# Kernel tuning notes

Hardware: AMD Instinct MI355X
Metric: run time of the kernel (lower is better)

Reference implementation:

```python
import jax, jax.numpy as jnp
import numpy as np

LN_EPS = 1e-5        # torch default LayerNorm eps
DEB_EPS = 1e-7       # deberta-v3 layer_norm_eps
ATT_SPAN = 256       # deberta-v3-base position_buckets -> pos_ebd_size
MAX_REL = 100        # config.max_relative_positions override


def _ln(x, g, b, eps):
    m = x.mean(-1, keepdims=True)
    v = jnp.var(x, axis=-1, keepdims=True)
    return (x - m) * jax.lax.rsqrt(v + eps) * g + b


def _lin(x, w, b):
    return x @ w.T + b


def _rel_buckets(L):
    # build_relative_position + make_log_bucket_position (bucket_size=256, max_position=100)
    rel = jnp.arange(L, dtype=jnp.int32)[:, None] - jnp.arange(L, dtype=jnp.int32)[None, :]
    mid = ATT_SPAN // 2
    sign = jnp.sign(rel)
    abs_pos = jnp.where((rel < mid) & (rel > -mid), mid - 1, jnp.abs(rel))
    log_pos = jnp.ceil(jnp.log(abs_pos.astype(jnp.float32) / mid)
                       / np.float32(np.log((MAX_REL - 1) / mid)) * (mid - 1)) + mid
    return jnp.where(abs_pos <= mid, rel, (log_pos * sign).astype(jnp.int32))


def _forward(ints, floats):
    type_ids, landmark_ids, mask = ints
    (xs, ys, zs, type_emb, landmark_emb, type_ln_g, type_ln_b, lm_ln_g, lm_ln_b,
     pos_w, pos_b, lt_in_w, lt_in_b, lt_out_w, lt_out_b, lt_ln1_g, lt_ln1_b,
     lt_ff1_w, lt_ff1_b, lt_ff2_w, lt_ff2_b, lt_ln2_g, lt_ln2_b,
     rel_emb, rel_ln_g, rel_ln_b, dq_w, dq_b, dk_w, dk_b, dv_w, dv_b,
     dao_w, dao_b, da_ln_g, da_ln_b, di_w, di_b, do_w, do_b, do_ln_g, do_ln_b,
     head_w, head_b) = floats

    # embeddings (padding_idx=0 -> zero row & zero grad) + layernorms + pos projection
    te = _ln(type_emb[type_ids] * (type_ids != 0)[..., None].astype(jnp.float32), type_ln_g, type_ln_b, LN_EPS)
    le = _ln(landmark_emb[landmark_ids] * (landmark_ids != 0)[..., None].astype(jnp.float32), lm_ln_g, lm_ln_b, LN_EPS)
    pe = _lin(jnp.stack([xs, ys, zs], -1), pos_w, pos_b)
    fts = jnp.concatenate([te, le, pe], -1)                  # [B,F,L,768]
    B, F, L, D = fts.shape
    h = fts.reshape(B * F, L, D)

    # --- nn.TransformerEncoderLayer over landmarks (post-norm, relu, nhead=1) ---
    q, k, v = jnp.split(_lin(h, lt_in_w, lt_in_b), 3, axis=-1)
    probs = jax.nn.softmax(jnp.einsum('bqd,bkd->bqk', q, k) / np.float32(np.sqrt(D)), axis=-1)
    attn = _lin(jnp.einsum('bqk,bkd->bqd', probs, v), lt_out_w, lt_out_b)
    h = _ln(h + attn, lt_ln1_g, lt_ln1_b, LN_EPS)
    ff = _lin(jax.nn.relu(_lin(h, lt_ff1_w, lt_ff1_b)), lt_ff2_w, lt_ff2_b)
    h = _ln(h + ff, lt_ln2_g, lt_ln2_b, LN_EPS)

    h = h.reshape(B, F, L, D).mean(2)                        # [B,F,768]

    # --- DebertaV2 layer over frames (disentangled attention, 1 head) ---
    m = mask[:, :, 0] > 0                                    # [B,F]
    q = _lin(h, dq_w, dq_b)
    k = _lin(h, dk_w, dk_b)
    v = _lin(h, dv_w, dv_b)
    scale = np.float32(np.sqrt(D * 3))                       # scale_factor = 1 + len({c2p,p2c})
    scores = jnp.einsum('bqd,bkd->bqk', q, k) / scale
    rel_ln = _ln(rel_emb, rel_ln_g, rel_ln_b, DEB_EPS)       # norm_rel_ebd='layer_norm'
    pos_q = _lin(rel_ln, dq_w, dq_b)                         # share_att_key=True
    pos_k = _lin(rel_ln, dk_w, dk_b)
    rel = _rel_buckets(F)                                    # [F,F]
    c2p_idx = jnp.clip(rel + ATT_SPAN, 0, 2 * ATT_SPAN - 1)
    c2p = jnp.einsum('bqd,rd->bqr', q, pos_k)                # [B,F,512]
    c2p = jnp.take_along_axis(c2p, jnp.broadcast_to(c2p_idx[None], (B, F, F)), axis=-1)
    p2c_idx = jnp.clip(-rel + ATT_SPAN, 0, 2 * ATT_SPAN - 1)
    p2c = jnp.einsum('bkd,rd->bkr', k, pos_q)                # [B,F,512]
    p2c = jnp.take_along_axis(p2c, jnp.broadcast_to(p2c_idx[None], (B, F, F)), axis=-1)
    scores = scores + (c2p + jnp.swapaxes(p2c, -1, -2)) / scale
    amask = m[:, :, None] & m[:, None, :]                    # XSoftmax mask
    probs = jax.nn.softmax(jnp.where(amask, scores, jnp.finfo(scores.dtype).min), axis=-1)
    probs = jnp.where(amask, probs, 0.0)
    ctx = jnp.einsum('bqk,bkd->bqd', probs, v)
    h = _ln(_lin(ctx, dao_w, dao_b) + h, da_ln_g, da_ln_b, DEB_EPS)
    inter = jax.nn.gelu(_lin(h, di_w, di_b), approximate=False)
    h = _ln(_lin(inter, do_w, do_b) + h, do_ln_g, do_ln_b, DEB_EPS)

    return _lin(h.mean(1), head_w, head_b)                   # [B,250]


def setup_inputs():
    ks = iter(jax.random.split(jax.random.key(0), 64))
    B, F, L, E, D, DF, NC = 8, 80, 100, 256, 768, 3072, 250
    def w(*shape):
        return jax.random.normal(next(ks), shape, dtype=jnp.float32) * 0.02
    z = lambda *s: jnp.zeros(s, jnp.float32)
    o = lambda *s: jnp.ones(s, jnp.float32)
    return {
        "type_ids": jax.random.randint(next(ks), (B, F, L), 0, 12, dtype=jnp.int32),
        "landmark_ids": jax.random.randint(next(ks), (B, F, L), 0, 127, dtype=jnp.int32),
        "xs": jax.random.normal(next(ks), (B, F, L), dtype=jnp.float32),
        "ys": jax.random.normal(next(ks), (B, F, L), dtype=jnp.float32),
        "zs": jax.random.normal(next(ks), (B, F, L), dtype=jnp.float32),
        "mask": jnp.ones((B, F, L), jnp.int32),
        "type_emb": w(12, E), "landmark_emb": w(127, E),
        "type_ln_g": o(E), "type_ln_b": z(E), "lm_ln_g": o(E), "lm_ln_b": z(E),
        "pos_w": w(E, 3), "pos_b": z(E),
        "lt_in_w": w(3 * D, D), "lt_in_b": z(3 * D), "lt_out_w": w(D, D), "lt_out_b": z(D),
        "lt_ln1_g": o(D), "lt_ln1_b": z(D),
        "lt_ff1_w": w(D, D), "lt_ff1_b": z(D), "lt_ff2_w": w(D, D), "lt_ff2_b": z(D),
        "lt_ln2_g": o(D), "lt_ln2_b": z(D),
        "rel_emb": w(2 * ATT_SPAN, D), "rel_ln_g": o(D), "rel_ln_b": z(D),
        "dq_w": w(D, D), "dq_b": z(D), "dk_w": w(D, D), "dk_b": z(D), "dv_w": w(D, D), "dv_b": z(D),
        "dao_w": w(D, D), "dao_b": z(D), "da_ln_g": o(D), "da_ln_b": z(D),
        "di_w": w(DF, D), "di_b": z(DF), "do_w": w(D, DF), "do_b": z(D),
        "do_ln_g": o(D), "do_ln_b": z(D),
        "head_w": w(NC, D), "head_b": z(NC),
    }


def reference(type_ids, landmark_ids, xs, ys, zs, mask, type_emb, landmark_emb,
              type_ln_g, type_ln_b, lm_ln_g, lm_ln_b, pos_w, pos_b,
              lt_in_w, lt_in_b, lt_out_w, lt_out_b, lt_ln1_g, lt_ln1_b,
              lt_ff1_w, lt_ff1_b, lt_ff2_w, lt_ff2_b, lt_ln2_g, lt_ln2_b,
              rel_emb, rel_ln_g, rel_ln_b, dq_w, dq_b, dk_w, dk_b, dv_w, dv_b,
              dao_w, dao_b, da_ln_g, da_ln_b, di_w, di_b, do_w, do_b,
              do_ln_g, do_ln_b, head_w, head_b):
    floats = (xs, ys, zs, type_emb, landmark_emb, type_ln_g, type_ln_b, lm_ln_g, lm_ln_b,
              pos_w, pos_b, lt_in_w, lt_in_b, lt_out_w, lt_out_b, lt_ln1_g, lt_ln1_b,
              lt_ff1_w, lt_ff1_b, lt_ff2_w, lt_ff2_b, lt_ln2_g, lt_ln2_b,
              rel_emb, rel_ln_g, rel_ln_b, dq_w, dq_b, dk_w, dk_b, dv_w, dv_b,
              dao_w, dao_b, da_ln_g, da_ln_b, di_w, di_b, do_w, do_b, do_ln_g, do_ln_b,
              head_w, head_b)
    return _forward((type_ids, landmark_ids, mask), floats)
```

## Files before the change

kernel.cpp:

```cpp
#include <hip/hip_runtime.h>

using short8v = __attribute__((ext_vector_type(8))) short;
using float4v = __attribute__((ext_vector_type(4))) float;

__device__ __forceinline__ unsigned short f2bf(float f) {
  unsigned int u = __float_as_uint(f);
  u += 0x7FFF + ((u >> 16) & 1);
  return (unsigned short)(u >> 16);
}
__device__ __forceinline__ float bf2f(unsigned short u) {
  return __uint_as_float((unsigned int)u << 16);
}

__device__ __forceinline__ int swz(int row, int c) {
  return row * 64 + (c ^ ((row & 7) << 3));
}

template<int BM, int ACT, bool OUTBF, int RES>
__global__ __launch_bounds__(256) void gemm_mfma(
    const unsigned short* __restrict__ A, const unsigned short* __restrict__ B,
    const float* __restrict__ bias, const void* __restrict__ resid, int ldr,
    void* __restrict__ Cv,
    int M, int N, int K, int lda, int ldb, int ldc,
    long long sA, long long sB, long long sC, long long sBias, float alpha)
{
  constexpr int NF = BM / 32;
  A += (long long)blockIdx.z * sA;
  B += (long long)blockIdx.z * sB;
  if (bias) bias += (long long)blockIdx.z * sBias;
  const int m0 = blockIdx.y * BM, n0 = blockIdx.x * BM;

  __shared__ __align__(16) unsigned short As[BM * 64];
  __shared__ __align__(16) unsigned short Bs[BM * 64];

  const int tid = threadIdx.x;
  const int w = tid >> 6, lane = tid & 63;
  const int wr = w >> 1, wc = w & 1;

  const int r0 = tid >> 3;
  const int c8 = (tid & 7) * 8;
  int ra[NF], rb[NF], soff[NF];
  #pragma unroll
  for (int i = 0; i < NF; ++i) {
    int r = m0 + r0 + i * 32; ra[i] = r < M - 1 ? r : M - 1;
    int q = n0 + r0 + i * 32; rb[i] = q < N - 1 ? q : N - 1;
    soff[i] = swz(r0 + i * 32, c8);
  }

  const int fr = lane & 15;
  const int fk = (lane >> 4) * 8;

  float4v acc[NF][NF] = {};

  short8v pa[NF], pb[NF];
  #pragma unroll
  for (int i = 0; i < NF; ++i) {
    pa[i] = *(const short8v*)(A + (long long)ra[i] * lda + c8);
    pb[i] = *(const short8v*)(B + (long long)rb[i] * ldb + c8);
  }

  for (int k0 = 0; k0 < K; k0 += 64) {
    __syncthreads();
    #pragma unroll
    for (int i = 0; i < NF; ++i) {
      *(short8v*)&As[soff[i]] = pa[i];
      *(short8v*)&Bs[soff[i]] = pb[i];
    }
    __syncthreads();
    if (k0 + 64 < K) {
      #pragma unroll
      for (int i = 0; i < NF; ++i) {
        pa[i] = *(const short8v*)(A + (long long)ra[i] * lda + k0 + 64 + c8);
        pb[i] = *(const short8v*)(B + (long long)rb[i] * ldb + k0 + 64 + c8);
      }
    }
    #pragma unroll
    for (int kk = 0; kk < 2; ++kk) {
      short8v a[NF], b[NF];
      #pragma unroll
      for (int i = 0; i < NF; ++i) {
        a[i] = *(const short8v*)&As[swz(wr * (NF * 16) + i * 16 + fr, kk * 32 + fk)];
        b[i] = *(const short8v*)&Bs[swz(wc * (NF * 16) + i * 16 + fr, kk * 32 + fk)];
      }
      #pragma unroll
      for (int mi = 0; mi < NF; ++mi)
        #pragma unroll
        for (int ni = 0; ni < NF; ++ni)
          acc[mi][ni] = __builtin_amdgcn_mfma_f32_16x16x32_bf16(a[mi], b[ni], acc[mi][ni], 0, 0, 0);
    }
  }

  const int ccol0 = n0 + wc * (NF * 16) + (lane & 15);
  const int crow0 = m0 + wr * (NF * 16) + (lane >> 4) * 4;
  float* Cf = (float*)Cv + (long long)blockIdx.z * sC;
  unsigned short* Cb = (unsigned short*)Cv + (long long)blockIdx.z * sC;
  #pragma unroll
  for (int ni = 0; ni < NF; ++ni) {
    const int col = ccol0 + ni * 16;
    if (col >= N) continue;
    const float bs = bias ? bias[col] : 0.f;
    #pragma unroll
    for (int mi = 0; mi < NF; ++mi) {
      #pragma unroll
      for (int r = 0; r < 4; ++r) {
        const int row = crow0 + mi * 16 + r;
        if (row >= M) continue;
        float v = acc[mi][ni][r] * alpha + bs;
        if (RES == 1) v += bf2f(((const unsigned short*)resid)[(long long)row * ldr + col]);
        if (RES == 2) v += ((const float*)resid)[(long long)row * ldr + col];
        if (ACT == 1) v = fmaxf(v, 0.f);
        if (ACT == 2) v = 0.5f * v * (1.f + erff(v * 0.70710678118654752f));
        if (OUTBF) Cb[(long long)row * ldc + col] = f2bf(v);
        else       Cf[(long long)row * ldc + col] = v;
      }
    }
  }
}

static void mg(hipStream_t st, int bm, int act, bool outbf, int res,
               const unsigned short* A, const unsigned short* B,
               const float* bias, const void* resid, int ldr, void* C,
               int M, int N, int K, int lda, int ldb, int ldc,
               long long sA, long long sB, long long sC, long long sBias,
               int bat, float alpha)
{
  dim3 grid((N + bm - 1) / bm, (M + bm - 1) / bm, bat);
  dim3 blk(256);
  #define GEMM_CALL(BM_, A_, O_, R_) \
    gemm_mfma<BM_, A_, O_, R_><<<grid, blk, 0, st>>>(A, B, bias, resid, ldr, C, \
        M, N, K, lda, ldb, ldc, sA, sB, sC, sBias, alpha)
  if (bm == 128) {
    if (outbf) {
      if (act == 1)       GEMM_CALL(128, 1, true, 0);
      else if (res == 1)  GEMM_CALL(128, 0, true, 1);
      else                GEMM_CALL(128, 0, true, 0);
    } else {
      GEMM_CALL(128, 0, false, 0);
    }
  } else {
    if (outbf) {
      if (act == 2)       GEMM_CALL(64, 2, true, 0);
      else                GEMM_CALL(64, 0, true, 0);
    } else {
      if (res == 2)       GEMM_CALL(64, 0, false, 2);
      else                GEMM_CALL(64, 0, false, 0);
    }
  }
  #undef GEMM_CALL
}

template<int MODE>
__global__ __launch_bounds__(256) void attn_fused(
    const unsigned short* __restrict__ Q, const unsigned short* __restrict__ Kp,
    const unsigned short* __restrict__ VT,
    const float* __restrict__ c2p, const float* __restrict__ p2c,
    const int* __restrict__ mask,
    unsigned short* __restrict__ O,
    int Mv, int K, int lda, int ldvt, int ldc,
    long long sQ, long long sVT, long long sO, float alpha)
{
  const int z = blockIdx.z;
  Q  += (long long)z * sQ;
  Kp += (long long)z * sQ;
  VT += (long long)z * sVT;
  O  += (long long)z * sO;

  __shared__ __align__(16) unsigned short As[128 * 64];
  __shared__ __align__(16) unsigned short Bs[128 * 64];
  __shared__ __align__(16) unsigned short Pl[128 * 128];
  float* ovl = (float*)As;
  int*   smk = (int*)(ovl + 512);

  const int tid = threadIdx.x;
  const int w = tid >> 6, lane = tid & 63;
  const int wr = w >> 1, wc = w & 1;
  const int r0 = tid >> 3, c8 = (tid & 7) * 8;

  int ra[4], soff[4];
  #pragma unroll
  for (int i = 0; i < 4; ++i) {
    int r = r0 + i * 32;
    ra[i] = (r < Mv - 1 ? r : Mv - 1);
    soff[i] = swz(r, c8);
  }
  const int fr = lane & 15, fk = (lane >> 4) * 8;

  float4v acc[4][4] = {};
  short8v pa[4], pb[4];
  #pragma unroll
  for (int i = 0; i < 4; ++i) {
    pa[i] = *(const short8v*)(Q  + (long long)ra[i] * lda + c8);
    pb[i] = *(const short8v*)(Kp + (long long)ra[i] * lda + c8);
  }
  for (int k0 = 0; k0 < K; k0 += 64) {
    __syncthreads();
    #pragma unroll
    for (int i = 0; i < 4; ++i) {
      *(short8v*)&As[soff[i]] = pa[i];
      *(short8v*)&Bs[soff[i]] = pb[i];
    }
    __syncthreads();
    if (k0 + 64 < K) {
      #pragma unroll
      for (int i = 0; i < 4; ++i) {
        pa[i] = *(const short8v*)(Q  + (long long)ra[i] * lda + k0 + 64 + c8);
        pb[i] = *(const short8v*)(Kp + (long long)ra[i] * lda + k0 + 64 + c8);
      }
    }
    #pragma unroll
    for (int kk = 0; kk < 2; ++kk) {
      short8v a[4], b[4];
      #pragma unroll
      for (int i = 0; i < 4; ++i) {
        a[i] = *(const short8v*)&As[swz(wr * 64 + i * 16 + fr, kk * 32 + fk)];
        b[i] = *(const short8v*)&Bs[swz(wc * 64 + i * 16 + fr, kk * 32 + fk)];
      }
      #pragma unroll
      for (int mi = 0; mi < 4; ++mi)
        #pragma unroll
        for (int ni = 0; ni < 4; ++ni)
          acc[mi][ni] = __builtin_amdgcn_mfma_f32_16x16x32_bf16(a[mi], b[ni], acc[mi][ni], 0, 0, 0);
    }
  }

  __syncthreads();
  if (MODE == 3 && tid < 80) smk[tid] = mask[((long long)z * 80 + tid) * 100];
  __syncthreads();

  const int g = lane >> 4, f = lane & 15;
  const int colB = wc * 64 + f;
  const int rowB = wr * 64 + g * 4;

  bool cv[4];
  #pragma unroll
  for (int ni = 0; ni < 4; ++ni) {
    const int col = colB + ni * 16;
    cv[ni] = (MODE == 2) ? (col < Mv) : (col < 80 && smk[col] != 0);
  }

  float lm[4][4];
  #pragma unroll
  for (int mi = 0; mi < 4; ++mi) {
    #pragma unroll
    for (int r = 0; r < 4; ++r) {
      const int row = rowB + mi * 16 + r;
      const bool rv = (MODE == 2) ? true : (row < 80 && smk[row] != 0);
      float mx = -3.4e38f;
      #pragma unroll
      for (int ni = 0; ni < 4; ++ni) {
        float v = acc[mi][ni][r] * alpha;
        const int col = colB + ni * 16;
        const bool valid = rv && cv[ni];
        if (MODE == 3 && valid) {
          const int rr = 256 + row - col;
          v += (c2p[((long long)z * 80 + row) * 512 + rr] +
                p2c[((long long)z * 80 + col) * 512 + rr]) * alpha;
        }
        v = valid ? v : -3.4e38f;
        acc[mi][ni][r] = v;
        mx = fmaxf(mx, v);
      }
      #pragma unroll
      for (int off = 1; off < 16; off <<= 1) mx = fmaxf(mx, __shfl_xor(mx, off, 64));
      lm[mi][r] = mx;
    }
  }
  if (f == 0) {
    #pragma unroll
    for (int mi = 0; mi < 4; ++mi)
      #pragma unroll
      for (int r = 0; r < 4; ++r)
        ovl[wc * 128 + rowB + mi * 16 + r] = lm[mi][r];
  }
  __syncthreads();
  float ls[4][4], mfin[4][4];
  #pragma unroll
  for (int mi = 0; mi < 4; ++mi) {
    #pragma unroll
    for (int r = 0; r < 4; ++r) {
      const int row = rowB + mi * 16 + r;
      const float m = fmaxf(lm[mi][r], ovl[(wc ^ 1) * 128 + row]);
      mfin[mi][r] = m;
      float s = 0.f;
      #pragma unroll
      for (int ni = 0; ni < 4; ++ni) {
        const float v = acc[mi][ni][r];
        const float e = (v > -1e37f) ? expf(v - m) : 0.f;
        acc[mi][ni][r] = e;
        s += e;
      }
      #pragma unroll
      for (int off = 1; off < 16; off <<= 1) s += __shfl_xor(s, off, 64);
      ls[mi][r] = s;
    }
  }
  if (f == 0) {
    #pragma unroll
    for (int mi = 0; mi < 4; ++mi)
      #pragma unroll
      for (int r = 0; r < 4; ++r)
        ovl[256 + wc * 128 + rowB + mi * 16 + r] = ls[mi][r];
  }
  __syncthreads();
  #pragma unroll
  for (int mi = 0; mi < 4; ++mi) {
    #pragma unroll
    for (int r = 0; r < 4; ++r) {
      const int row = rowB + mi * 16 + r;
      const float tot = ls[mi][r] + ovl[256 + (wc ^ 1) * 128 + row];
      const float inv = (tot > 0.f) ? 1.f / tot : 0.f;
      #pragma unroll
      for (int ni = 0; ni < 4; ++ni) {
        const int col = colB + ni * 16;
        Pl[row * 128 + (col ^ ((row & 7) << 3))] = f2bf(acc[mi][ni][r] * inv);
      }
    }
  }
  __syncthreads();

  for (int n0 = 0; n0 < 768; n0 += 128) {
    short8v v0[4], v1[4];
    #pragma unroll
    for (int i = 0; i < 4; ++i) {
      const int rv = n0 + r0 + i * 32;
      v0[i] = *(const short8v*)(VT + (long long)rv * ldvt + c8);
      v1[i] = *(const short8v*)(VT + (long long)rv * ldvt + 64 + c8);
    }
    __syncthreads();
    #pragma unroll
    for (int i = 0; i < 4; ++i) {
      *(short8v*)&As[soff[i]] = v0[i];
      *(short8v*)&Bs[soff[i]] = v1[i];
    }
    __syncthreads();

    float4v oacc[4][4] = {};
    #pragma unroll
    for (int half = 0; half < 2; ++half) {
      const unsigned short* src = half ? Bs : As;
      #pragma unroll
      for (int kk = 0; kk < 2; ++kk) {
        const int kglob = half * 64 + kk * 32 + fk;
        short8v a[4], b[4];
        #pragma unroll
        for (int i = 0; i < 4; ++i) {
          const int prow = wr * 64 + i * 16 + fr;
          a[i] = *(const short8v*)&Pl[prow * 128 + (kglob ^ ((prow & 7) << 3))];
          b[i] = *(const short8v*)&src[swz(wc * 64 + i * 16 + fr, kk * 32 + fk)];
        }
        #pragma unroll
        for (int mi = 0; mi < 4; ++mi)
          #pragma unroll
          for (int ni = 0; ni < 4; ++ni)
            oacc[mi][ni] = __builtin_amdgcn_mfma_f32_16x16x32_bf16(a[mi], b[ni], oacc[mi][ni], 0, 0, 0);
      }
    }
    #pragma unroll
    for (int ni = 0; ni < 4; ++ni) {
      const int col = n0 + colB + ni * 16;
      #pragma unroll
      for (int mi = 0; mi < 4; ++mi) {
        #pragma unroll
        for (int r = 0; r < 4; ++r) {
          const int row = rowB + mi * 16 + r;
          if (row < Mv) O[(long long)row * ldc + col] = f2bf(oacc[mi][ni][r]);
        }
      }
    }
  }
}

struct ConvArgs {
  const float* s[10];
  unsigned short* d[10];
  long long off[11];
};
__global__ __launch_bounds__(256) void convall_kernel(ConvArgs a, long long tot)
{
  const long long i = ((long long)blockIdx.x * 256 + threadIdx.x) * 4;
  if (i >= tot) return;
  int t = 0;
  while (i >= a.off[t + 1]) ++t;
  const long long j = i - a.off[t];
  const float4 v = *(const float4*)(a.s[t] + j);
  const unsigned int lo = (unsigned int)f2bf(v.x) | ((unsigned int)f2bf(v.y) << 16);
  const unsigned int hi = (unsigned int)f2bf(v.z) | ((unsigned int)f2bf(v.w) << 16);
  *(uint2*)(a.d[t] + j) = make_uint2(lo, hi);
}

__global__ __launch_bounds__(256) void embed_kernel(
    const int* __restrict__ tids, const int* __restrict__ lids,
    const float* __restrict__ xs, const float* __restrict__ ys, const float* __restrict__ zs,
    const float* __restrict__ temb, const float* __restrict__ lemb,
    const float* __restrict__ tg, const float* __restrict__ tb,
    const float* __restrict__ lg, const float* __restrict__ lb,
    const float* __restrict__ pw, const float* __restrict__ pb,
    unsigned short* __restrict__ hb)
{
  const int tok = blockIdx.x * 4 + (threadIdx.x >> 6);
  const int lane = threadIdx.x & 63;
  const int e0 = lane * 4;
  const int ti = tids[tok], li = lids[tok];
  float4 tv = make_float4(0.f, 0.f, 0.f, 0.f);
  float4 lv = make_float4(0.f, 0.f, 0.f, 0.f);
  if (ti != 0) tv = *(const float4*)(temb + ti * 256 + e0);
  if (li != 0) lv = *(const float4*)(lemb + li * 256 + e0);

  float s0 = tv.x + tv.y + tv.z + tv.w;
  float s1 = tv.x * tv.x + tv.y * tv.y + tv.z * tv.z + tv.w * tv.w;
  float s2 = lv.x + lv.y + lv.z + lv.w;
  float s3 = lv.x * lv.x + lv.y * lv.y + lv.z * lv.z + lv.w * lv.w;
  #pragma unroll
  for (int off = 32; off > 0; off >>= 1) {
    s0 += __shfl_xor(s0, off, 64);
    s1 += __shfl_xor(s1, off, 64);
    s2 += __shfl_xor(s2, off, 64);
    s3 += __shfl_xor(s3, off, 64);
  }
  const float mt = s0 * (1.f / 256.f), vt = s1 * (1.f / 256.f) - mt * mt;
  const float ml = s2 * (1.f / 256.f), vl = s3 * (1.f / 256.f) - ml * ml;
  const float rt = rsqrtf(vt + 1e-5f), rl = rsqrtf(vl + 1e-5f);

  const float4 tg4 = *(const float4*)(tg + e0), tb4 = *(const float4*)(tb + e0);
  const float4 lg4 = *(const float4*)(lg + e0), lb4 = *(const float4*)(lb + e0);
  const size_t base = (size_t)tok * 768;
  ushort4 o;
  o.x = f2bf((tv.x - mt) * rt * tg4.x + tb4.x);
  o.y = f2bf((tv.y - mt) * rt * tg4.y + tb4.y);
  o.z = f2bf((tv.z - mt) * rt * tg4.z + tb4.z);
  o.w = f2bf((tv.w - mt) * rt * tg4.w + tb4.w);
  *(ushort4*)(hb + base + e0) = o;
  o.x = f2bf((lv.x - ml) * rl * lg4.x + lb4.x);
  o.y = f2bf((lv.y - ml) * rl * lg4.y + lb4.y);
  o.z = f2bf((lv.z - ml) * rl * lg4.z + lb4.z);
  o.w = f2bf((lv.w - ml) * rl * lg4.w + lb4.w);
  *(ushort4*)(hb + base + 256 + e0) = o;

  const float X = xs[tok], Y = ys[tok], Z = zs[tok];
  const float4 w0 = *(const float4*)(pw + 12 * lane);
  const float4 w1 = *(const float4*)(pw + 12 * lane + 4);
  const float4 w2 = *(const float4*)(pw + 12 * lane + 8);
  const float4 pb4 = *(const float4*)(pb + e0);
  o.x = f2bf(w0.x * X + w0.y * Y + w0.z * Z + pb4.x);
  o.y = f2bf(w0.w * X + w1.x * Y + w1.y * Z + pb4.y);
  o.z = f2bf(w1.z * X + w1.w * Y + w2.x * Z + pb4.z);
  o.w = f2bf(w2.y * X + w2.z * Y + w2.w * Z + pb4.w);
  *(ushort4*)(hb + base + 512 + e0) = o;
}

template<int XBF, int RBF>
__global__ __launch_bounds__(256) void ln_kernel(
    const void* __restrict__ x, const void* __restrict__ res,
    const float* __restrict__ g, const float* __restrict__ b,
    float* __restrict__ yf, unsigned short* __restrict__ yb,
    int nrows, float eps)
{
  const int row = blockIdx.x * 4 + (threadIdx.x >> 6);
  if (row >= nrows) return;
  const int lane = threadIdx.x & 63;
  const size_t base = (size_t)row * 768;
  const int e0 = lane * 12;
  float v[12];
  #pragma unroll
  for (int j = 0; j < 3; ++j) {
    if (XBF) {
      const ushort4 u = *(const ushort4*)((const unsigned short*)x + base + e0 + 4 * j);
      v[4*j+0] = bf2f(u.x); v[4*j+1] = bf2f(u.y); v[4*j+2] = bf2f(u.z); v[4*j+3] = bf2f(u.w);
    } else {
      const float4 fx = *(const float4*)((const float*)x + base + e0 + 4 * j);
      v[4*j+0] = fx.x; v[4*j+1] = fx.y; v[4*j+2] = fx.z; v[4*j+3] = fx.w;
    }
  }
  if (res) {
    #pragma unroll
    for (int j = 0; j < 3; ++j) {
      if (RBF) {
        const ushort4 u = *(const ushort4*)((const unsigned short*)res + base + e0 + 4 * j);
        v[4*j+0] += bf2f(u.x); v[4*j+1] += bf2f(u.y); v[4*j+2] += bf2f(u.z); v[4*j+3] += bf2f(u.w);
      } else {
        const float4 fx = *(const float4*)((const float*)res + base + e0 + 4 * j);
        v[4*j+0] += fx.x; v[4*j+1] += fx.y; v[4*j+2] += fx.z; v[4*j+3] += fx.w;
      }
    }
  }
  float s = 0.f, ss = 0.f;
  #pragma unroll
  for (int j = 0; j < 12; ++j) { s += v[j]; ss += v[j] * v[j]; }
  #pragma unroll
  for (int off = 32; off > 0; off >>= 1) {
    s += __shfl_xor(s, off, 64);
    ss += __shfl_xor(ss, off, 64);
  }
  const float mean = s * (1.f / 768.f);
  const float rstd = rsqrtf(ss * (1.f / 768.f) - mean * mean + eps);
  #pragma unroll
  for (int j = 0; j < 3; ++j) {
    const float4 g4 = *(const float4*)(g + e0 + 4 * j);
    const float4 b4 = *(const float4*)(b + e0 + 4 * j);
    float o0 = (v[4*j+0] - mean) * rstd * g4.x + b4.x;
    float o1 = (v[4*j+1] - mean) * rstd * g4.y + b4.y;
    float o2 = (v[4*j+2] - mean) * rstd * g4.z + b4.z;
    float o3 = (v[4*j+3] - mean) * rstd * g4.w + b4.w;
    if (yf) *(float4*)(yf + base + e0 + 4 * j) = make_float4(o0, o1, o2, o3);
    if (yb) {
      ushort4 u; u.x = f2bf(o0); u.y = f2bf(o1); u.z = f2bf(o2); u.w = f2bf(o3);
      *(ushort4*)(yb + base + e0 + 4 * j) = u;
    }
  }
}

__global__ __launch_bounds__(256) void vtrans_kernel(
    const unsigned short* __restrict__ v, unsigned short* __restrict__ vt,
    int Lk, int rs, long long sIn, long long sOut)
{
  __shared__ unsigned short s[64][132];
  const int b = blockIdx.y, d0 = blockIdx.x * 64;
  const unsigned short* vb = v + (long long)b * sIn;
  unsigned short* ob = vt + (long long)b * sOut;
  for (int idx = threadIdx.x; idx < 128 * 64; idx += 256) {
    const int k = idx >> 6, dd = idx & 63;
    s[dd][k] = (k < Lk) ? vb[(long long)k * rs + d0 + dd] : (unsigned short)0;
  }
  __syncthreads();
  for (int idx = threadIdx.x; idx < 64 * 128; idx += 256) {
    const int dd = idx >> 7, k = idx & 127;
    ob[(long long)(d0 + dd) * 128 + k] = s[dd][k];
  }
}

__global__ __launch_bounds__(192) void meanL_kernel(
    const unsigned short* __restrict__ hb, float* __restrict__ hf,
    unsigned short* __restrict__ hfb)
{
  const int bf = blockIdx.x;
  const int d0 = threadIdx.x * 4;
  float4 acc = make_float4(0.f, 0.f, 0.f, 0.f);
  for (int l = 0; l < 100; ++l) {
    const ushort4 u = *(const ushort4*)(hb + ((size_t)bf * 100 + l) * 768 + d0);
    acc.x += bf2f(u.x); acc.y += bf2f(u.y); acc.z += bf2f(u.z); acc.w += bf2f(u.w);
  }
  acc.x *= 0.01f; acc.y *= 0.01f; acc.z *= 0.01f; acc.w *= 0.01f;
  *(float4*)(hf + (size_t)bf * 768 + d0) = acc;
  ushort4 o; o.x = f2bf(acc.x); o.y = f2bf(acc.y); o.z = f2bf(acc.z); o.w = f2bf(acc.w);
  *(ushort4*)(hfb + (size_t)bf * 768 + d0) = o;
}

__global__ __launch_bounds__(192) void meanF_kernel(const float* __restrict__ h4, float* __restrict__ hm)
{
  const int b = blockIdx.x;
  const int d0 = threadIdx.x * 4;
  float4 acc = make_float4(0.f, 0.f, 0.f, 0.f);
  for (int f = 0; f < 80; ++f) {
    const float4 u = *(const float4*)(h4 + ((size_t)b * 80 + f) * 768 + d0);
    acc.x += u.x; acc.y += u.y; acc.z += u.z; acc.w += u.w;
  }
  const float k = 1.f / 80.f;
  *(float4*)(hm + (size_t)b * 768 + d0) = make_float4(acc.x * k, acc.y * k, acc.z * k, acc.w * k);
}

__global__ __launch_bounds__(64) void head_kernel(
    const float* __restrict__ hm, const float* __restrict__ w,
    const float* __restrict__ bias, float* __restrict__ out)
{
  const int n = blockIdx.x, b = blockIdx.y;
  const float* x = hm + (size_t)b * 768;
  const float* wn = w + (size_t)n * 768;
  float s = 0.f;
  for (int i = threadIdx.x * 4; i < 768; i += 256) {
    const float4 xv = *(const float4*)(x + i);
    const float4 wv = *(const float4*)(wn + i);
    s += xv.x * wv.x + xv.y * wv.y + xv.z * wv.z + xv.w * wv.w;
  }
  #pragma unroll
  for (int off = 32; off > 0; off >>= 1) s += __shfl_down(s, off, 64);
  if (threadIdx.x == 0) out[(size_t)b * 250 + n] = s + bias[n];
}

extern "C" void kernel_launch(void* const* d_in, const int* in_sizes, int n_in,
                              void* d_out, int out_size, void* d_ws, size_t ws_size,
                              hipStream_t stream)
{
  const int*   type_ids   = (const int*)  d_in[0];
  const int*   lm_ids     = (const int*)  d_in[1];
  const float* xs         = (const float*)d_in[2];
  const float* ys         = (const float*)d_in[3];
  const float* zs         = (const float*)d_in[4];
  const int*   mask       = (const int*)  d_in[5];
  const float* type_emb   = (const float*)d_in[6];
  const float* lm_emb     = (const float*)d_in[7];
  const float* type_ln_g  = (const float*)d_in[8];
  const float* type_ln_b  = (const float*)d_in[9];
  const float* lm_ln_g    = (const float*)d_in[10];
  const float* lm_ln_b    = (const float*)d_in[11];
  const float* pos_w      = (const float*)d_in[12];
  const float* pos_b      = (const float*)d_in[13];
  const float* lt_in_w    = (const float*)d_in[14];
  const float* lt_in_b    = (const float*)d_in[15];
  const float* lt_out_w   = (const float*)d_in[16];
  const float* lt_out_b   = (const float*)d_in[17];
  const float* lt_ln1_g   = (const float*)d_in[18];
  const float* lt_ln1_b   = (const float*)d_in[19];
  const float* lt_ff1_w   = (const float*)d_in[20];
  const float* lt_ff1_b   = (const float*)d_in[21];
  const float* lt_ff2_w   = (const float*)d_in[22];
  const float* lt_ff2_b   = (const float*)d_in[23];
  const float* lt_ln2_g   = (const float*)d_in[24];
  const float* lt_ln2_b   = (const float*)d_in[25];
  const float* rel_emb    = (const float*)d_in[26];
  const float* rel_ln_g   = (const float*)d_in[27];
  const float* rel_ln_b   = (const float*)d_in[28];
  const float* dq_w       = (const float*)d_in[29];
  const float* dq_b       = (const float*)d_in[30];
  const float* dk_w       = (const float*)d_in[31];
  const float* dk_b       = (const float*)d_in[32];
  const float* dv_w       = (const float*)d_in[33];
  const float* dv_b       = (const float*)d_in[34];
  const float* dao_w      = (const float*)d_in[35];
  const float* dao_b      = (const float*)d_in[36];
  const float* da_ln_g    = (const float*)d_in[37];
  const float* da_ln_b    = (const float*)d_in[38];
  const float* di_w       = (const float*)d_in[39];
  const float* di_b       = (const float*)d_in[40];
  const float* do_w       = (const float*)d_in[41];
  const float* do_b       = (const float*)d_in[42];
  const float* do_ln_g    = (const float*)d_in[43];
  const float* do_ln_b    = (const float*)d_in[44];
  const float* head_w     = (const float*)d_in[45];
  const float* head_b     = (const float*)d_in[46];
  float* out = (float*)d_out;
  float* ws  = (float*)d_ws;

  const float inv_sqrt_d = 0.03608439182435161f;
  const long long W2 = 768 * 768;

  auto rnd = [](size_t x) { return (x + 63) & ~(size_t)63; };
  const size_t ws_floats = ws_size / sizeof(float);

  size_t o = 0;
  const size_t offHB = o; o += rnd((size_t)64000 * 768 / 2);
  auto woff = [&](size_t elems) { size_t r = o; o += rnd(elems / 2); return r; };
  const size_t w_in   = woff((size_t)2304 * 768);
  const size_t w_out  = woff((size_t)768 * 768);
  const size_t w_f1   = woff((size_t)768 * 768);
  const size_t w_f2   = woff((size_t)768 * 768);
  const size_t w_qkv3 = woff((size_t)2304 * 768);
  const size_t w_ao   = woff((size_t)768 * 768);
  const size_t w_di   = woff((size_t)3072 * 768);
  const size_t w_do   = woff((size_t)768 * 3072);
  const size_t b_qkv3 = o; o += rnd(2304);
  const size_t scratch0 = o;

  size_t s3need = 0;
  {
    size_t t = 0;
    t += rnd((size_t)640 * 768);
    t += rnd((size_t)1152 * 768 / 2);
    t += rnd((size_t)1152 * 2304 / 2);
    t += 2 * (size_t)640 * 512;
    t += rnd((size_t)8 * 98304 / 2);
    t += rnd((size_t)640 * 768 / 2);
    t += 2 * rnd((size_t)640 * 768);
    t += rnd((size_t)640 * 768 / 2);
    t += rnd((size_t)640 * 3072 / 2);
    t += 2 * rnd((size_t)640 * 768);
    t += rnd((size_t)8 * 768);
    s3need = t;
  }

  auto chunk_need = [&](int c) {
    const size_t R = (size_t)c * 100;
    size_t t = 0;
    t += rnd(R * 2304 / 2);
    t += 4 * rnd(R * 768 / 2);
    t += rnd((size_t)c * 98304 / 2);
    return t;
  };
  int C = 1;
  {
    const int cands[] = {640, 320, 160, 80, 40, 20, 10, 5, 2, 1};
    for (int c : cands) {
      const size_t need = scratch0 + (chunk_need(c) > s3need ? chunk_need(c) : s3need);
      if (need <= ws_floats) { C = c; break; }
    }
  }
  const size_t R = (size_t)C * 100;

  o = scratch0;
  const size_t qkvb = o; o += rnd(R * 2304 / 2);
  const size_t ctxb = o; o += rnd(R * 768 / 2);
  const size_t t1b  = o; o += rnd(R * 768 / 2);
  const size_t h1bb = o; o += rnd(R * 768 / 2);
  const size_t ffob = o; o += rnd(R * 768 / 2);
  const size_t vtb  = o; o += rnd((size_t)C * 98304 / 2);

  auto US = [&](size_t foff) { return (unsigned short*)(ws + foff); };

  {
    ConvArgs a;
    const float* srcs[10] = {lt_in_w, lt_out_w, lt_ff1_w, lt_ff2_w,
                             dq_w, dk_w, dv_w, dao_w, di_w, do_w};
    unsigned short* dsts[10] = {US(w_in), US(w_out), US(w_f1), US(w_f2),
                                US(w_qkv3), US(w_qkv3) + W2, US(w_qkv3) + 2 * W2,
                                US(w_ao), US(w_di), US(w_do)};
    const long long ns[10] = {2304 * 768, W2, W2, W2, W2, W2, W2, W2,
                              3072 * 768, 3072 * 768};
    long long tot = 0;
    for (int i = 0; i < 10; ++i) { a.s[i] = srcs[i]; a.d[i] = dsts[i]; a.off[i] = tot; tot += ns[i]; }
    a.off[10] = tot;
    convall_kernel<<<(unsigned)((tot / 4 + 255) / 256), 256, 0, stream>>>(a, tot);
  }
  hipMemcpyAsync(ws + b_qkv3,        dq_b, 768 * sizeof(float), hipMemcpyDeviceToDevice, stream);
  hipMemcpyAsync(ws + b_qkv3 + 768,  dk_b, 768 * sizeof(float), hipMemcpyDeviceToDevice, stream);
  hipMemcpyAsync(ws + b_qkv3 + 1536, dv_b, 768 * sizeof(float), hipMemcpyDeviceToDevice, stream);

  embed_kernel<<<16000, 256, 0, stream>>>(type_ids, lm_ids, xs, ys, zs,
      type_emb, lm_emb, type_ln_g, type_ln_b, lm_ln_g, lm_ln_b, pos_w, pos_b,
      US(offHB));

  for (int c0 = 0; c0 < 640; c0 += C) {
    unsigned short* hbc = US(offHB) + (size_t)c0 * 100 * 768;
    const int Rr = C * 100;
    mg(stream, 128, 0, true, 0, hbc, US(w_in), lt_in_b, nullptr, 0, US(qkvb),
       Rr, 2304, 768, 768, 768, 2304, 0, 0, 0, 0, 1, 1.f);
    vtrans_kernel<<<dim3(12, C), 256, 0, stream>>>(US(qkvb) + 1536, US(vtb), 100, 2304, 230400, 98304);
    attn_fused<2><<<dim3(1, 1, C), 256, 0, stream>>>(
        US(qkvb), US(qkvb) + 768, US(vtb), nullptr, nullptr, nullptr, US(ctxb),
        100, 768, 2304, 128, 768, 230400, 98304, 76800, inv_sqrt_d);
    mg(stream, 128, 0, true, 1, US(ctxb), US(w_out), lt_out_b, hbc, 768, US(t1b),
       Rr, 768, 768, 768, 768, 768, 0, 0, 0, 0, 1, 1.f);
    ln_kernel<1, 1><<<(Rr + 3) / 4, 256, 0, stream>>>(US(t1b), nullptr,
        lt_ln1_g, lt_ln1_b, nullptr, US(h1bb), Rr, 1e-5f);
    mg(stream, 128, 1, true, 0, US(h1bb), US(w_f1), lt_ff1_b, nullptr, 0, US(ffob),
       Rr, 768, 768, 768, 768, 768, 0, 0, 0, 0, 1, 1.f);
    mg(stream, 128, 0, true, 1, US(ffob), US(w_f2), lt_ff2_b, US(h1bb), 768, US(t1b),
       Rr, 768, 768, 768, 768, 768, 0, 0, 0, 0, 1, 1.f);
    ln_kernel<1, 1><<<(Rr + 3) / 4, 256, 0, stream>>>(US(t1b), nullptr,
        lt_ln2_g, lt_ln2_b, nullptr, hbc, Rr, 1e-5f);
  }

  o = scratch0;
  const size_t hf    = o; o += rnd((size_t)640 * 768);
  const size_t hfbE  = o; o += rnd((size_t)1152 * 768 / 2);
  const size_t qp    = o; o += rnd((size_t)1152 * 2304 / 2);
  const size_t c2p   = o; o += (size_t)640 * 512;
  const size_t p2c   = o; o += (size_t)640 * 512;
  const size_t vt3b  = o; o += rnd((size_t)8 * 98304 / 2);
  const size_t ctx3b = o; o += rnd((size_t)640 * 768 / 2);
  const size_t t3    = o; o += rnd((size_t)640 * 768);
  const size_t h3    = o; o += rnd((size_t)640 * 768);
  const size_t h3b   = o; o += rnd((size_t)640 * 768 / 2);
  const size_t interb= o; o += rnd((size_t)640 * 3072 / 2);
  const size_t t4    = o; o += rnd((size_t)640 * 768);
  const size_t h4    = o; o += rnd((size_t)640 * 768);
  const size_t hm    = o; o += rnd((size_t)8 * 768);

  meanL_kernel<<<640, 192, 0, stream>>>(US(offHB), ws + hf, US(hfbE));
  ln_kernel<0, 0><<<128, 256, 0, stream>>>(rel_emb, nullptr,
      rel_ln_g, rel_ln_b, nullptr, US(hfbE) + (size_t)640 * 768, 512, 1e-7f);
  mg(stream, 64, 0, true, 0, US(hfbE), US(w_qkv3), ws + b_qkv3, nullptr, 0, US(qp),
     1152, 2304, 768, 768, 768, 2304, 0, 0, 0, 0, 1, 1.f);
  mg(stream, 64, 0, false, 0, US(qp), US(qp) + (size_t)640 * 2304 + 768, nullptr, nullptr, 0, ws + c2p,
     640, 512, 768, 2304, 2304, 512, 768, -768, 327680, 0, 2, 1.f);
  vtrans_kernel<<<dim3(12, 8), 256, 0, stream>>>(US(qp) + 1536, US(vt3b), 80, 2304, 184320, 98304);
  attn_fused<3><<<dim3(1, 1, 8), 256, 0, stream>>>(
      US(qp), US(qp) + 768, US(vt3b), ws + c2p, ws + p2c, mask, US(ctx3b),
      80, 768, 2304, 128, 768, 184320, 98304, 61440, 1.f / 48.f);
  mg(stream, 64, 0, false, 2, US(ctx3b), US(w_ao), dao_b, ws + hf, 768, ws + t3,
     640, 768, 768, 768, 768, 768, 0, 0, 0, 0, 1, 1.f);
  ln_kernel<0, 0><<<160, 256, 0, stream>>>(ws + t3, nullptr,
      da_ln_g, da_ln_b, ws + h3, US(h3b), 640, 1e-7f);
  mg(stream, 64, 2, true, 0, US(h3b), US(w_di), di_b, nullptr, 0, US(interb),
     640, 3072, 768, 768, 768, 3072, 0, 0, 0, 0, 1, 1.f);
  mg(stream, 64, 0, false, 2, US(interb), US(w_do), do_b, ws + h3, 768, ws + t4,
     640, 768, 3072, 3072, 3072, 768, 0, 0, 0, 0, 1, 1.f);
  ln_kernel<0, 0><<<160, 256, 0, stream>>>(ws + t4, nullptr,
      do_ln_g, do_ln_b, ws + h4, nullptr, 640, 1e-7f);
  meanF_kernel<<<8, 192, 0, stream>>>(ws + h4, ws + hm);
  head_kernel<<<dim3(250, 8), 64, 0, stream>>>(ws + hm, head_w, head_b, out);
}
```

Baseline: 2.171 ms.

## Split fused attention into score-softmax kernel plus batched GEMM for PV

Replaces the single-block-per-batch fused attention kernel with a separate score+softmax kernel that writes bf16 probabilities, followed by the generic tiled GEMM for probs×V. The disentangled attention path likewise becomes a batched QK GEMM, a small per-row masked softmax kernel with c2p/p2c bias, and a GEMM for the context. The aim is to spread the PV product (768 output columns) across many blocks instead of looping serially inside one block per batch. The cost is extra launches and round-trips of scores and probabilities through global memory.

New measurement: 1.950 ms, median of 2. 1.11x faster.

```diff
diff --git a/kernel.cpp b/kernel.cpp
--- a/kernel.cpp
+++ b/kernel.cpp
@@ -149,27 +149,19 @@
   #undef GEMM_CALL
 }
 
-template<int MODE>
-__global__ __launch_bounds__(256) void attn_fused(
+__global__ __launch_bounds__(256) void scoresm_kernel(
     const unsigned short* __restrict__ Q, const unsigned short* __restrict__ Kp,
-    const unsigned short* __restrict__ VT,
-    const float* __restrict__ c2p, const float* __restrict__ p2c,
-    const int* __restrict__ mask,
-    unsigned short* __restrict__ O,
-    int Mv, int K, int lda, int ldvt, int ldc,
-    long long sQ, long long sVT, long long sO, float alpha)
+    unsigned short* __restrict__ P,
+    int Mv, int K, int lda, long long sQ, long long sP, float alpha)
 {
   const int z = blockIdx.z;
   Q  += (long long)z * sQ;
   Kp += (long long)z * sQ;
-  VT += (long long)z * sVT;
-  O  += (long long)z * sO;
+  P  += (long long)z * sP;
 
   __shared__ __align__(16) unsigned short As[128 * 64];
   __shared__ __align__(16) unsigned short Bs[128 * 64];
-  __shared__ __align__(16) unsigned short Pl[128 * 128];
   float* ovl = (float*)As;
-  int*   smk = (int*)(ovl + 512);
 
   const int tid = threadIdx.x;
   const int w = tid >> 6, lane = tid & 63;
@@ -222,9 +214,6 @@
           acc[mi][ni] = __builtin_amdgcn_mfma_f32_16x16x32_bf16(a[mi], b[ni], acc[mi][ni], 0, 0, 0);
     }
   }
-
-  __syncthreads();
-  if (MODE == 3 && tid < 80) smk[tid] = mask[((long long)z * 80 + tid) * 100];
   __syncthreads();
 
   const int g = lane >> 4, f = lane & 15;
@@ -233,30 +222,17 @@
 
   bool cv[4];
   #pragma unroll
-  for (int ni = 0; ni < 4; ++ni) {
-    const int col = colB + ni * 16;
-    cv[ni] = (MODE == 2) ? (col < Mv) : (col < 80 && smk[col] != 0);
-  }
+  for (int ni = 0; ni < 4; ++ni) cv[ni] = (colB + ni * 16) < Mv;
 
   float lm[4][4];
   #pragma unroll
   for (int mi = 0; mi < 4; ++mi) {
     #pragma unroll
     for (int r = 0; r < 4; ++r) {
-      const int row = rowB + mi * 16 + r;
-      const bool rv = (MODE == 2) ? true : (row < 80 && smk[row] != 0);
       float mx = -3.4e38f;
       #pragma unroll
       for (int ni = 0; ni < 4; ++ni) {
-        float v = acc[mi][ni][r] * alpha;
-        const int col = colB + ni * 16;
-        const bool valid = rv && cv[ni];
-        if (MODE == 3 && valid) {
-          const int rr = 256 + row - col;
-          v += (c2p[((long long)z * 80 + row) * 512 + rr] +
-                p2c[((long long)z * 80 + col) * 512 + rr]) * alpha;
-        }
-        v = valid ? v : -3.4e38f;
+        float v = cv[ni] ? acc[mi][ni][r] * alpha : -3.4e38f;
         acc[mi][ni][r] = v;
         mx = fmaxf(mx, v);
       }
@@ -273,14 +249,13 @@
         ovl[wc * 128 + rowB + mi * 16 + r] = lm[mi][r];
   }
   __syncthreads();
-  float ls[4][4], mfin[4][4];
+  float ls[4][4];
   #pragma unroll
   for (int mi = 0; mi < 4; ++mi) {
     #pragma unroll
     for (int r = 0; r < 4; ++r) {
       const int row = rowB + mi * 16 + r;
       const float m = fmaxf(lm[mi][r], ovl[(wc ^ 1) * 128 + row]);
-      mfin[mi][r] = m;
       float s = 0.f;
       #pragma unroll
       for (int ni = 0; ni < 4; ++ni) {
@@ -310,62 +285,8 @@
       const float tot = ls[mi][r] + ovl[256 + (wc ^ 1) * 128 + row];
       const float inv = (tot > 0.f) ? 1.f / tot : 0.f;
       #pragma unroll
-      for (int ni = 0; ni < 4; ++ni) {
-        const int col = colB + ni * 16;
-        Pl[row * 128 + (col ^ ((row & 7) << 3))] = f2bf(acc[mi][ni][r] * inv);
-      }
-    }
-  }
-  __syncthreads();
-
-  for (int n0 = 0; n0 < 768; n0 += 128) {
-    short8v v0[4], v1[4];
-    #pragma unroll
-    for (int i = 0; i < 4; ++i) {
-      const int rv = n0 + r0 + i * 32;
-      v0[i] = *(const short8v*)(VT + (long long)rv * ldvt + c8);
-      v1[i] = *(const short8v*)(VT + (long long)rv * ldvt + 64 + c8);
-    }
-    __syncthreads();
-    #pragma unroll
-    for (int i = 0; i < 4; ++i) {
-      *(short8v*)&As[soff[i]] = v0[i];
-      *(short8v*)&Bs[soff[i]] = v1[i];
-    }
-    __syncthreads();
-
-    float4v oacc[4][4] = {};
-    #pragma unroll
-    for (int half = 0; half < 2; ++half) {
-      const unsigned short* src = half ? Bs : As;
-      #pragma unroll
-      for (int kk = 0; kk < 2; ++kk) {
-        const int kglob = half * 64 + kk * 32 + fk;
-        short8v a[4], b[4];
-        #pragma unroll
-        for (int i = 0; i < 4; ++i) {
-          const int prow = wr * 64 + i * 16 + fr;
-          a[i] = *(const short8v*)&Pl[prow * 128 + (kglob ^ ((prow & 7) << 3))];
-          b[i] = *(const short8v*)&src[swz(wc * 64 + i * 16 + fr, kk * 32 + fk)];
-        }
-        #pragma unroll
-        for (int mi = 0; mi < 4; ++mi)
-          #pragma unroll
-          for (int ni = 0; ni < 4; ++ni)
-            oacc[mi][ni] = __builtin_amdgcn_mfma_f32_16x16x32_bf16(a[mi], b[ni], oacc[mi][ni], 0, 0, 0);
-      }
-    }
-    #pragma unroll
-    for (int ni = 0; ni < 4; ++ni) {
-      const int col = n0 + colB + ni * 16;
-      #pragma unroll
-      for (int mi = 0; mi < 4; ++mi) {
-        #pragma unroll
-        for (int r = 0; r < 4; ++r) {
-          const int row = rowB + mi * 16 + r;
-          if (row < Mv) O[(long long)row * ldc + col] = f2bf(oacc[mi][ni][r]);
-        }
-      }
+      for (int ni = 0; ni < 4; ++ni)
+        P[(long long)row * 128 + colB + ni * 16] = f2bf(acc[mi][ni][r] * inv);
     }
   }
 }
@@ -526,6 +447,52 @@
     const int dd = idx >> 7, k = idx & 127;
     ob[(long long)(d0 + dd) * 128 + k] = s[dd][k];
   }
+}
+
+__global__ __launch_bounds__(256) void deb3_kernel(
+    const float* __restrict__ sc,
+    const float* __restrict__ c2p,
+    const float* __restrict__ p2c,
+    const int* __restrict__ mask,
+    unsigned short* __restrict__ probs)
+{
+  const int rid = blockIdx.x * 4 + (threadIdx.x >> 6);
+  if (rid >= 640) return;
+  const int b = rid / 80, q = rid - b * 80;
+  const int lane = threadIdx.x & 63;
+  const bool mq = mask[(size_t)rid * 100] > 0;
+  float v0 = -3.4e38f, v1 = -3.4e38f;
+  bool val0 = false, val1 = false;
+  {
+    const int k = lane;
+    const bool mk = mask[(size_t)(b * 80 + k) * 100] > 0;
+    val0 = mq && mk;
+    const int r = 256 + q - k;
+    if (val0)
+      v0 = sc[(size_t)b * 16384 + (size_t)q * 128 + k] +
+           (c2p[(size_t)rid * 512 + r] + p2c[(size_t)(b * 80 + k) * 512 + r]) * (1.f / 48.f);
+  }
+  if (lane + 64 < 80) {
+    const int k = lane + 64;
+    const bool mk = mask[(size_t)(b * 80 + k) * 100] > 0;
+    val1 = mq && mk;
+    const int r = 256 + q - k;
+    if (val1)
+      v1 = sc[(size_t)b * 16384 + (size_t)q * 128 + k] +
+           (c2p[(size_t)rid * 512 + r] + p2c[(size_t)(b * 80 + k) * 512 + r]) * (1.f / 48.f);
+  }
+  float m = fmaxf(v0, v1);
+  #pragma unroll
+  for (int off = 32; off > 0; off >>= 1) m = fmaxf(m, __shfl_xor(m, off, 64));
+  const float e0 = val0 ? expf(v0 - m) : 0.f;
+  const float e1 = val1 ? expf(v1 - m) : 0.f;
+  float s = e0 + e1;
+  #pragma unroll
+  for (int off = 32; off > 0; off >>= 1) s += __shfl_xor(s, off, 64);
+  const float inv = (s > 0.f) ? 1.f / s : 0.f;
+  unsigned short* orow = probs + (size_t)b * 16384 + (size_t)q * 128;
+  orow[lane] = val0 ? f2bf(e0 * inv) : (unsigned short)0;
+  orow[lane + 64] = val1 ? f2bf(e1 * inv) : (unsigned short)0;
 }
 
 __global__ __launch_bounds__(192) void meanL_kernel(
@@ -657,6 +624,8 @@
     t += rnd((size_t)1152 * 768 / 2);
     t += rnd((size_t)1152 * 2304 / 2);
     t += 2 * (size_t)640 * 512;
+    t += rnd((size_t)8 * 16384);
+    t += rnd((size_t)8 * 16384 / 2);
     t += rnd((size_t)8 * 98304 / 2);
     t += rnd((size_t)640 * 768 / 2);
     t += 2 * rnd((size_t)640 * 768);
@@ -673,6 +642,7 @@
     t += rnd(R * 2304 / 2);
     t += 4 * rnd(R * 768 / 2);
     t += rnd((size_t)c * 98304 / 2);
+    t += rnd((size_t)c * 16384 / 2);
     return t;
   };
   int C = 1;
@@ -692,6 +662,7 @@
   const size_t h1bb = o; o += rnd(R * 768 / 2);
   const size_t ffob = o; o += rnd(R * 768 / 2);
   const size_t vtb  = o; o += rnd((size_t)C * 98304 / 2);
+  const size_t pbf  = o; o += rnd((size_t)C * 16384 / 2);
 
   auto US = [&](size_t foff) { return (unsigned short*)(ws + foff); };
 
@@ -722,10 +693,11 @@
     const int Rr = C * 100;
     mg(stream, 128, 0, true, 0, hbc, US(w_in), lt_in_b, nullptr, 0, US(qkvb),
        Rr, 2304, 768, 768, 768, 2304, 0, 0, 0, 0, 1, 1.f);
+    scoresm_kernel<<<dim3(1, 1, C), 256, 0, stream>>>(
+        US(qkvb), US(qkvb) + 768, US(pbf), 100, 768, 2304, 230400, 16384, inv_sqrt_d);
     vtrans_kernel<<<dim3(12, C), 256, 0, stream>>>(US(qkvb) + 1536, US(vtb), 100, 2304, 230400, 98304);
-    attn_fused<2><<<dim3(1, 1, C), 256, 0, stream>>>(
-        US(qkvb), US(qkvb) + 768, US(vtb), nullptr, nullptr, nullptr, US(ctxb),
-        100, 768, 2304, 128, 768, 230400, 98304, 76800, inv_sqrt_d);
+    mg(stream, 128, 0, true, 0, US(pbf), US(vtb), nullptr, nullptr, 0, US(ctxb),
+       100, 768, 128, 128, 128, 768, 16384, 98304, 76800, 0, C, 1.f);
     mg(stream, 128, 0, true, 1, US(ctxb), US(w_out), lt_out_b, hbc, 768, US(t1b),
        Rr, 768, 768, 768, 768, 768, 0, 0, 0, 0, 1, 1.f);
     ln_kernel<1, 1><<<(Rr + 3) / 4, 256, 0, stream>>>(US(t1b), nullptr,
@@ -744,6 +716,8 @@
   const size_t qp    = o; o += rnd((size_t)1152 * 2304 / 2);
   const size_t c2p   = o; o += (size_t)640 * 512;
   const size_t p2c   = o; o += (size_t)640 * 512;
+  const size_t p32_3 = o; o += rnd((size_t)8 * 16384);
+  const size_t p3bf  = o; o += rnd((size_t)8 * 16384 / 2);
   const size_t vt3b  = o; o += rnd((size_t)8 * 98304 / 2);
   const size_t ctx3b = o; o += rnd((size_t)640 * 768 / 2);
   const size_t t3    = o; o += rnd((size_t)640 * 768);
@@ -759,12 +733,14 @@
       rel_ln_g, rel_ln_b, nullptr, US(hfbE) + (size_t)640 * 768, 512, 1e-7f);
   mg(stream, 64, 0, true, 0, US(hfbE), US(w_qkv3), ws + b_qkv3, nullptr, 0, US(qp),
      1152, 2304, 768, 768, 768, 2304, 0, 0, 0, 0, 1, 1.f);
+  mg(stream, 64, 0, false, 0, US(qp), US(qp) + 768, nullptr, nullptr, 0, ws + p32_3,
+     80, 80, 768, 2304, 2304, 128, 184320, 184320, 16384, 0, 8, 1.f / 48.f);
   mg(stream, 64, 0, false, 0, US(qp), US(qp) + (size_t)640 * 2304 + 768, nullptr, nullptr, 0, ws + c2p,
      640, 512, 768, 2304, 2304, 512, 768, -768, 327680, 0, 2, 1.f);
+  deb3_kernel<<<160, 256, 0, stream>>>(ws + p32_3, ws + c2p, ws + p2c, mask, US(p3bf));
   vtrans_kernel<<<dim3(12, 8), 256, 0, stream>>>(US(qp) + 1536, US(vt3b), 80, 2304, 184320, 98304);
-  attn_fused<3><<<dim3(1, 1, 8), 256, 0, stream>>>(
-      US(qp), US(qp) + 768, US(vt3b), ws + c2p, ws + p2c, mask, US(ctx3b),
-      80, 768, 2304, 128, 768, 184320, 98304, 61440, 1.f / 48.f);
+  mg(stream, 64, 0, true, 0, US(p3bf), US(vt3b), nullptr, nullptr, 0, US(ctx3b),
+     80, 768, 128, 128, 128, 768, 16384, 98304, 61440, 0, 8, 1.f);
   mg(stream, 64, 0, false, 2, US(ctx3b), US(w_ao), dao_b, ws + hf, 768, ws + t3,
      640, 768, 768, 768, 768, 768, 0, 0, 0, 0, 1, 1.f);
   ln_kernel<0, 0><<<160, 256, 0, stream>>>(ws + t3, nullptr,
```
